# Optimization experiments

Hardware: AMD Instinct MI355X
Metric: run time of the kernel (lower is better)

Reference implementation:

```python
import jax, jax.numpy as jnp
import numpy as np

N, R, H0, H1, NB, E = 25000, 16, 256, 256, 16, 800000


def setup_inputs() -> dict:
    key = jax.random.key(0)
    ks = jax.random.split(key, 6)
    s = jax.random.randint(ks[0], (E,), 0, N)
    p = jax.random.randint(ks[1], (E,), 0, R)
    o = jax.random.randint(ks[2], (E,), 0, N)
    triples = jnp.stack([s, p, o], axis=1)  # (E, 3) int
    nodes = jax.random.normal(ks[3], (N, H0), dtype=jnp.float32)
    xav_c = (6.0 / (R + NB)) ** 0.5  # xavier-uniform scale proxy
    xav_b = (6.0 / (H0 + H1)) ** 0.5
    comps = jax.random.uniform(ks[4], (R, NB), dtype=jnp.float32, minval=-xav_c, maxval=xav_c)
    bases = jax.random.uniform(ks[5], (NB, H0, H1), dtype=jnp.float32, minval=-xav_b, maxval=xav_b)
    bias = jnp.zeros((H1,), dtype=jnp.float32)
    return {"triples": triples, "nodes": nodes, "comps": comps, "bases": bases, "bias": bias}


def reference(triples, nodes, comps, bases, bias):
    # RGCNLayer forward, hor=True, decomp='basis', insize given.
    s, p, o = triples[:, 0], triples[:, 1], triples[:, 2]
    e = s.shape[0]
    # Vertical adjacency row index (p*n + s); normalization = 1 / row-sum (sum_sparse)
    row_ver = p * N + s
    deg = jax.ops.segment_sum(jnp.ones((e,), dtype=nodes.dtype), row_ver, num_segments=R * N)
    vals = 1.0 / deg[row_ver]  # (E,) per-edge normalized value
    # Basis decomposition: weights (R, H0, H1)
    weights = jnp.einsum('rb,bij->rij', comps, bases)
    # Horizontal path: nw[r, n] = nodes @ W_r, then out = hor_adj @ nw.reshape(R*N, H1)
    nw = jnp.einsum('ni,rio->rno', nodes, weights)  # (R, N, H1)
    msgs = vals[:, None] * nw[p, o]  # (E, H1) gather of column blocks (p*n + o)
    out = jax.ops.segment_sum(msgs, s, num_segments=N)  # (N, H1) scatter into rows s
    return out + bias
```

## Files before the change

kernel.cpp:

```cpp
#include <hip/hip_runtime.h>
#include <hip/hip_bf16.h>

#define NN 25000
#define RR 16
#define H0 256
#define H1 256
#define NBASE 16
#define EE 800000
#define NKEY (NN*RR)
#define NKEY_PAD 400384
#define SCAN_NB 391

#define BM 32
#define CAPE 2048

static const size_t CNT_OFF  = 0;
static const size_t CUR_OFF  = 1601536;
static const size_t OFFS_OFF = 3203072;
static const size_t PART_OFF = 4804608;
static const size_t PERM_OFF = 4806656;
static const size_t W2_OFF   = 8006656;

typedef short bf16x8 __attribute__((ext_vector_type(8)));
typedef float f32x4  __attribute__((ext_vector_type(4)));

static __device__ __forceinline__ unsigned short f2bf(float f) {
    union { float f; unsigned u; } v; v.f = f;
    unsigned x = v.u;
    return (unsigned short)((x + 0x7FFFu + ((x >> 16) & 1u)) >> 16);
}

__global__ __launch_bounds__(256) void k_weights(const float* __restrict__ comps,
                                                 const float* __restrict__ bases,
                                                 unsigned short* __restrict__ W2) {
    __shared__ float sc[RR * NBASE];
    int t = threadIdx.x;
    sc[t] = comps[t];
    __syncthreads();
    int i = blockIdx.x;
    int j = t;
    int ij = i * 256 + j;
    float bv[NBASE];
#pragma unroll
    for (int b = 0; b < NBASE; ++b) bv[b] = bases[b * H0 * H1 + ij];
    int ks = i >> 5, u = i & 7, lq = (i >> 3) & 3;
    int nb = j >> 4, ln = j & 15;
#pragma unroll
    for (int r = 0; r < RR; ++r) {
        float acc = 0.f;
#pragma unroll
        for (int b = 0; b < NBASE; ++b) acc = fmaf(sc[r * NBASE + b], bv[b], acc);
        size_t sidx = (((size_t)(r * 8 + ks) * 16 + nb) * 64 + lq * 16 + ln) * 8 + u;
        W2[sidx] = f2bf(acc);
    }
}

__global__ __launch_bounds__(256) void k_cnt(const int* __restrict__ triples,
                                             int* __restrict__ cnt) {
    int e = blockIdx.x * 256 + threadIdx.x;
    if (e >= EE) return;
    int s = triples[3 * e];
    int p = triples[3 * e + 1];
    atomicAdd(&cnt[s * RR + p], 1);
}

__global__ __launch_bounds__(256) void k_scan1(const int* __restrict__ cnt,
                                               int* __restrict__ part) {
    __shared__ int sh[256];
    int t = threadIdx.x;
    int4 v = *(const int4*)(cnt + blockIdx.x * 1024 + t * 4);
    sh[t] = v.x + v.y + v.z + v.w;
    __syncthreads();
    for (int off = 128; off > 0; off >>= 1) {
        if (t < off) sh[t] += sh[t + off];
        __syncthreads();
    }
    if (t == 0) part[blockIdx.x] = sh[0];
}

__global__ void k_scan2(int* __restrict__ part) {
    __shared__ int sh[512];
    int t = threadIdx.x;
    sh[t] = (t < SCAN_NB) ? part[t] : 0;
    __syncthreads();
    for (int off = 1; off < 512; off <<= 1) {
        int v = (t >= off) ? sh[t - off] : 0;
        __syncthreads();
        sh[t] += v;
        __syncthreads();
    }
    if (t < SCAN_NB) part[t] = (t ? sh[t - 1] : 0);
}

__global__ __launch_bounds__(256) void k_scan3(const int* __restrict__ cnt,
                                               const int* __restrict__ part,
                                               int* __restrict__ offs) {
    __shared__ int sh[256];
    int t = threadIdx.x;
    int base = blockIdx.x * 1024 + t * 4;
    int4 v = *(const int4*)(cnt + base);
    sh[t] = v.x + v.y + v.z + v.w;
    __syncthreads();
    for (int off = 1; off < 256; off <<= 1) {
        int x = (t >= off) ? sh[t - off] : 0;
        __syncthreads();
        sh[t] += x;
        __syncthreads();
    }
    int texcl = part[blockIdx.x] + (t ? sh[t - 1] : 0);
    int4 w;
    w.x = texcl;
    w.y = texcl + v.x;
    w.z = texcl + v.x + v.y;
    w.w = texcl + v.x + v.y + v.z;
    *(int4*)(offs + base) = w;
}

__global__ __launch_bounds__(256) void k_fill(const int* __restrict__ triples,
                                              const int* __restrict__ offs,
                                              int* __restrict__ cur,
                                              int* __restrict__ perm_o) {
    int e = blockIdx.x * 256 + threadIdx.x;
    if (e >= EE) return;
    int s = triples[3 * e];
    int p = triples[3 * e + 1];
    int o = triples[3 * e + 2];
    int key = s * RR + p;
    int slot = offs[key] + atomicAdd(&cur[key], 1);
    perm_o[slot] = o;
}

__global__ __launch_bounds__(256, 4) void k_fused(const float* __restrict__ nodes,
                                                  const unsigned short* __restrict__ W2,
                                                  const int* __restrict__ offs,
                                                  const int* __restrict__ perm_o,
                                                  const float* __restrict__ bias,
                                                  float* __restrict__ out) {
    __shared__ int offs_l[BM * RR + 1];
    __shared__ int eo[CAPE];
    __shared__ unsigned short As[BM][264];

    int t = threadIdx.x;
    int l = t & 63;
    int w = t >> 6;
    int m0 = blockIdx.x * BM;
    int key0 = m0 * RR;

    for (int idx = t; idx < BM * RR + 1; idx += 256) {
        int g = key0 + idx;
        if (g > NKEY_PAD - 1) g = NKEY_PAD - 1;
        offs_l[idx] = offs[g];
    }
    __syncthreads();
    int base0 = offs_l[0];
    int span  = offs_l[BM * RR] - base0;
    for (int j = t; j < span && j < CAPE; j += 256) eo[j] = perm_o[base0 + j];
    __syncthreads();

    f32x4 acc[2][4];
#pragma unroll
    for (int mi = 0; mi < 2; ++mi)
#pragma unroll
        for (int ni = 0; ni < 4; ++ni) acc[mi][ni] = (f32x4){0.f, 0.f, 0.f, 0.f};

    for (int p = 0; p < RR; ++p) {
#pragma unroll
        for (int i = 0; i < 8; ++i) {
            int m = w * 8 + i;
            int s = m0 + m;
            float sx = 0.f, sy = 0.f, sz = 0.f, sw = 0.f;
            int c = 0;
            if (s < NN) {
                int loc = m * RR + p;
                int b = offs_l[loc] - base0;
                c = offs_l[loc + 1] - offs_l[loc];
                int j2 = 0;
                for (; j2 + 1 < c; j2 += 2) {
                    int x1 = b + j2, x2 = b + j2 + 1;
                    int o1 = (x1 < CAPE) ? eo[x1] : perm_o[base0 + x1];
                    int o2 = (x2 < CAPE) ? eo[x2] : perm_o[base0 + x2];
                    float4 v1 = *(const float4*)(nodes + (size_t)o1 * H0 + l * 4);
                    float4 v2 = *(const float4*)(nodes + (size_t)o2 * H0 + l * 4);
                    sx += v1.x + v2.x; sy += v1.y + v2.y;
                    sz += v1.z + v2.z; sw += v1.w + v2.w;
                }
                if (j2 < c) {
                    int x1 = b + j2;
                    int o1 = (x1 < CAPE) ? eo[x1] : perm_o[base0 + x1];
                    float4 v1 = *(const float4*)(nodes + (size_t)o1 * H0 + l * 4);
                    sx += v1.x; sy += v1.y; sz += v1.z; sw += v1.w;
                }
            }
            float inv = c ? 1.f / (float)c : 0.f;
            ushort4 pk;
            pk.x = f2bf(sx * inv); pk.y = f2bf(sy * inv);
            pk.z = f2bf(sz * inv); pk.w = f2bf(sw * inv);
            *(ushort4*)&As[m][l * 4] = pk;
        }
        __syncthreads();

        const unsigned short* Wp = W2 + (size_t)p * 65536;
#pragma unroll
        for (int ks = 0; ks < 8; ++ks) {
            int k0 = ks * 32;
            bf16x8 a0 = *(const bf16x8*)&As[(l & 15)][k0 + (l >> 4) * 8];
            bf16x8 a1 = *(const bf16x8*)&As[16 + (l & 15)][k0 + (l >> 4) * 8];
            const unsigned short* wb = Wp + ((size_t)ks * 16 + w * 4) * 512 + (size_t)l * 8;
            bf16x8 b0 = *(const bf16x8*)(wb);
            bf16x8 b1 = *(const bf16x8*)(wb + 512);
            bf16x8 b2 = *(const bf16x8*)(wb + 1024);
            bf16x8 b3 = *(const bf16x8*)(wb + 1536);
            acc[0][0] = __builtin_amdgcn_mfma_f32_16x16x32_bf16(a0, b0, acc[0][0], 0, 0, 0);
            acc[1][0] = __builtin_amdgcn_mfma_f32_16x16x32_bf16(a1, b0, acc[1][0], 0, 0, 0);
            acc[0][1] = __builtin_amdgcn_mfma_f32_16x16x32_bf16(a0, b1, acc[0][1], 0, 0, 0);
            acc[1][1] = __builtin_amdgcn_mfma_f32_16x16x32_bf16(a1, b1, acc[1][1], 0, 0, 0);
            acc[0][2] = __builtin_amdgcn_mfma_f32_16x16x32_bf16(a0, b2, acc[0][2], 0, 0, 0);
            acc[1][2] = __builtin_amdgcn_mfma_f32_16x16x32_bf16(a1, b2, acc[1][2], 0, 0, 0);
            acc[0][3] = __builtin_amdgcn_mfma_f32_16x16x32_bf16(a0, b3, acc[0][3], 0, 0, 0);
            acc[1][3] = __builtin_amdgcn_mfma_f32_16x16x32_bf16(a1, b3, acc[1][3], 0, 0, 0);
        }
        __syncthreads();
    }

    int colbase = w * 64 + (l & 15);
    float bl[4];
#pragma unroll
    for (int ni = 0; ni < 4; ++ni) bl[ni] = bias[colbase + ni * 16];
#pragma unroll
    for (int mi = 0; mi < 2; ++mi)
#pragma unroll
        for (int j = 0; j < 4; ++j) {
            int row = m0 + mi * 16 + (l >> 4) * 4 + j;
            if (row < NN) {
#pragma unroll
                for (int ni = 0; ni < 4; ++ni)
                    out[(size_t)row * H1 + colbase + ni * 16] = acc[mi][ni][j] + bl[ni];
            }
        }
}

extern "C" void kernel_launch(void* const* d_in, const int* in_sizes, int n_in,
                              void* d_out, int out_size, void* d_ws, size_t ws_size,
                              hipStream_t stream) {
    const int*   triples = (const int*)d_in[0];
    const float* nodes   = (const float*)d_in[1];
    const float* comps   = (const float*)d_in[2];
    const float* bases   = (const float*)d_in[3];
    const float* bias    = (const float*)d_in[4];
    float* out = (float*)d_out;

    char* ws = (char*)d_ws;
    int*            cnt    = (int*)(ws + CNT_OFF);
    int*            cur    = (int*)(ws + CUR_OFF);
    int*            offs   = (int*)(ws + OFFS_OFF);
    int*            part   = (int*)(ws + PART_OFF);
    int*            perm_o = (int*)(ws + PERM_OFF);
    unsigned short* W2     = (unsigned short*)(ws + W2_OFF);

    hipMemsetAsync(ws + CNT_OFF, 0, CUR_OFF + 1601536, stream);

    k_weights<<<256, 256, 0, stream>>>(comps, bases, W2);
    k_cnt<<<(EE + 255) / 256, 256, 0, stream>>>(triples, cnt);
    k_scan1<<<SCAN_NB, 256, 0, stream>>>(cnt, part);
    k_scan2<<<1, 512, 0, stream>>>(part);
    k_scan3<<<SCAN_NB, 256, 0, stream>>>(cnt, part, offs);
    k_fill<<<(EE + 255) / 256, 256, 0, stream>>>(triples, offs, cur, perm_o);
    k_fused<<<(NN + BM - 1) / BM, 256, 0, stream>>>(nodes, W2, offs, perm_o, bias, out);
}
```

Before: 357.7 us.

## Double-buffer aggregation with MFMA, halve row tile, reuse counts in fill

```diff
diff --git a/kernel.cpp b/kernel.cpp
--- a/kernel.cpp
+++ b/kernel.cpp
@@ -11,8 +11,8 @@
 #define NKEY_PAD 400384
 #define SCAN_NB 391
 
-#define BM 32
-#define CAPE 2048
+#define BM 16
+#define CAPE 1024
 
 static const size_t CNT_OFF  = 0;
 static const size_t CUR_OFF  = 1601536;
@@ -118,7 +118,7 @@
 
 __global__ __launch_bounds__(256) void k_fill(const int* __restrict__ triples,
                                               const int* __restrict__ offs,
-                                              int* __restrict__ cur,
+                                              int* __restrict__ cnt,
                                               int* __restrict__ perm_o) {
     int e = blockIdx.x * 256 + threadIdx.x;
     if (e >= EE) return;
@@ -126,11 +126,11 @@
     int p = triples[3 * e + 1];
     int o = triples[3 * e + 2];
     int key = s * RR + p;
-    int slot = offs[key] + atomicAdd(&cur[key], 1);
-    perm_o[slot] = o;
-}
-
-__global__ __launch_bounds__(256, 4) void k_fused(const float* __restrict__ nodes,
+    int r = atomicSub(&cnt[key], 1) - 1;
+    perm_o[offs[key] + r] = o;
+}
+
+__global__ __launch_bounds__(256, 6) void k_fused(const float* __restrict__ nodes,
                                                   const unsigned short* __restrict__ W2,
                                                   const int* __restrict__ offs,
                                                   const int* __restrict__ perm_o,
@@ -138,7 +138,7 @@
                                                   float* __restrict__ out) {
     __shared__ int offs_l[BM * RR + 1];
     __shared__ int eo[CAPE];
-    __shared__ unsigned short As[BM][264];
+    __shared__ unsigned short As[2][BM][264];
 
     int t = threadIdx.x;
     int l = t & 63;
@@ -155,18 +155,15 @@
     int base0 = offs_l[0];
     int span  = offs_l[BM * RR] - base0;
     for (int j = t; j < span && j < CAPE; j += 256) eo[j] = perm_o[base0 + j];
-    __syncthreads();
-
-    f32x4 acc[2][4];
-#pragma unroll
-    for (int mi = 0; mi < 2; ++mi)
-#pragma unroll
-        for (int ni = 0; ni < 4; ++ni) acc[mi][ni] = (f32x4){0.f, 0.f, 0.f, 0.f};
-
-    for (int p = 0; p < RR; ++p) {
-#pragma unroll
-        for (int i = 0; i < 8; ++i) {
-            int m = w * 8 + i;
+
+    f32x4 acc[4];
+#pragma unroll
+    for (int ni = 0; ni < 4; ++ni) acc[ni] = (f32x4){0.f, 0.f, 0.f, 0.f};
+
+    auto aggregate = [&](int p, int buf) {
+#pragma unroll
+        for (int i = 0; i < 4; ++i) {
+            int m = w * 4 + i;
             int s = m0 + m;
             float sx = 0.f, sy = 0.f, sz = 0.f, sw = 0.f;
             int c = 0;
@@ -195,29 +192,30 @@
             ushort4 pk;
             pk.x = f2bf(sx * inv); pk.y = f2bf(sy * inv);
             pk.z = f2bf(sz * inv); pk.w = f2bf(sw * inv);
-            *(ushort4*)&As[m][l * 4] = pk;
+            *(ushort4*)&As[buf][m][l * 4] = pk;
         }
-        __syncthreads();
-
+    };
+
+    __syncthreads();
+    aggregate(0, 0);
+    __syncthreads();
+
+    for (int p = 0; p < RR; ++p) {
+        if (p + 1 < RR) aggregate(p + 1, (p + 1) & 1);
+        int cb = p & 1;
         const unsigned short* Wp = W2 + (size_t)p * 65536;
 #pragma unroll
         for (int ks = 0; ks < 8; ++ks) {
-            int k0 = ks * 32;
-            bf16x8 a0 = *(const bf16x8*)&As[(l & 15)][k0 + (l >> 4) * 8];
-            bf16x8 a1 = *(const bf16x8*)&As[16 + (l & 15)][k0 + (l >> 4) * 8];
+            bf16x8 a0 = *(const bf16x8*)&As[cb][(l & 15)][ks * 32 + (l >> 4) * 8];
             const unsigned short* wb = Wp + ((size_t)ks * 16 + w * 4) * 512 + (size_t)l * 8;
             bf16x8 b0 = *(const bf16x8*)(wb);
             bf16x8 b1 = *(const bf16x8*)(wb + 512);
             bf16x8 b2 = *(const bf16x8*)(wb + 1024);
             bf16x8 b3 = *(const bf16x8*)(wb + 1536);
-            acc[0][0] = __builtin_amdgcn_mfma_f32_16x16x32_bf16(a0, b0, acc[0][0], 0, 0, 0);
-            acc[1][0] = __builtin_amdgcn_mfma_f32_16x16x32_bf16(a1, b0, acc[1][0], 0, 0, 0);
-            acc[0][1] = __builtin_amdgcn_mfma_f32_16x16x32_bf16(a0, b1, acc[0][1], 0, 0, 0);
-            acc[1][1] = __builtin_amdgcn_mfma_f32_16x16x32_bf16(a1, b1, acc[1][1], 0, 0, 0);
-            acc[0][2] = __builtin_amdgcn_mfma_f32_16x16x32_bf16(a0, b2, acc[0][2], 0, 0, 0);
-            acc[1][2] = __builtin_amdgcn_mfma_f32_16x16x32_bf16(a1, b2, acc[1][2], 0, 0, 0);
-            acc[0][3] = __builtin_amdgcn_mfma_f32_16x16x32_bf16(a0, b3, acc[0][3], 0, 0, 0);
-            acc[1][3] = __builtin_amdgcn_mfma_f32_16x16x32_bf16(a1, b3, acc[1][3], 0, 0, 0);
+            acc[0] = __builtin_amdgcn_mfma_f32_16x16x32_bf16(a0, b0, acc[0], 0, 0, 0);
+            acc[1] = __builtin_amdgcn_mfma_f32_16x16x32_bf16(a0, b1, acc[1], 0, 0, 0);
+            acc[2] = __builtin_amdgcn_mfma_f32_16x16x32_bf16(a0, b2, acc[2], 0, 0, 0);
+            acc[3] = __builtin_amdgcn_mfma_f32_16x16x32_bf16(a0, b3, acc[3], 0, 0, 0);
         }
         __syncthreads();
     }
@@ -227,16 +225,14 @@
 #pragma unroll
     for (int ni = 0; ni < 4; ++ni) bl[ni] = bias[colbase + ni * 16];
 #pragma unroll
-    for (int mi = 0; mi < 2; ++mi)
-#pragma unroll
-        for (int j = 0; j < 4; ++j) {
-            int row = m0 + mi * 16 + (l >> 4) * 4 + j;
-            if (row < NN) {
-#pragma unroll
-                for (int ni = 0; ni < 4; ++ni)
-                    out[(size_t)row * H1 + colbase + ni * 16] = acc[mi][ni][j] + bl[ni];
-            }
+    for (int j = 0; j < 4; ++j) {
+        int row = m0 + (l >> 4) * 4 + j;
+        if (row < NN) {
+#pragma unroll
+            for (int ni = 0; ni < 4; ++ni)
+                out[(size_t)row * H1 + colbase + ni * 16] = acc[ni][j] + bl[ni];
         }
+    }
 }
 
 extern "C" void kernel_launch(void* const* d_in, const int* in_sizes, int n_in,
@@ -251,19 +247,18 @@
 
     char* ws = (char*)d_ws;
     int*            cnt    = (int*)(ws + CNT_OFF);
-    int*            cur    = (int*)(ws + CUR_OFF);
     int*            offs   = (int*)(ws + OFFS_OFF);
     int*            part   = (int*)(ws + PART_OFF);
     int*            perm_o = (int*)(ws + PERM_OFF);
     unsigned short* W2     = (unsigned short*)(ws + W2_OFF);
 
-    hipMemsetAsync(ws + CNT_OFF, 0, CUR_OFF + 1601536, stream);
+    hipMemsetAsync(ws + CNT_OFF, 0, 1601536, stream);
 
     k_weights<<<256, 256, 0, stream>>>(comps, bases, W2);
     k_cnt<<<(EE + 255) / 256, 256, 0, stream>>>(triples, cnt);
     k_scan1<<<SCAN_NB, 256, 0, stream>>>(cnt, part);
     k_scan2<<<1, 512, 0, stream>>>(part);
     k_scan3<<<SCAN_NB, 256, 0, stream>>>(cnt, part, offs);
-    k_fill<<<(EE + 255) / 256, 256, 0, stream>>>(triples, offs, cur, perm_o);
+    k_fill<<<(EE + 255) / 256, 256, 0, stream>>>(triples, offs, cnt, perm_o);
     k_fused<<<(NN + BM - 1) / BM, 256, 0, stream>>>(nodes, W2, offs, perm_o, bias, out);
 }
```

Result: no change. 363.5 us (+1.6%).

## Gather bf16 node features, double-buffer aggregation tile, reuse counts for fill

Applied to the files above, without the earlier changes.

```diff
diff --git a/kernel.cpp b/kernel.cpp
--- a/kernel.cpp
+++ b/kernel.cpp
@@ -15,13 +15,14 @@
 #define CAPE 2048
 
 static const size_t CNT_OFF  = 0;
-static const size_t CUR_OFF  = 1601536;
-static const size_t OFFS_OFF = 3203072;
-static const size_t PART_OFF = 4804608;
-static const size_t PERM_OFF = 4806656;
-static const size_t W2_OFF   = 8006656;
+static const size_t OFFS_OFF = 1601536;
+static const size_t PART_OFF = 3203072;
+static const size_t PERM_OFF = 3205120;
+static const size_t W2_OFF   = 6405120;
+static const size_t NBF_OFF  = 8502272;
 
 typedef short bf16x8 __attribute__((ext_vector_type(8)));
+typedef short short8 __attribute__((ext_vector_type(8)));
 typedef float f32x4  __attribute__((ext_vector_type(4)));
 
 static __device__ __forceinline__ unsigned short f2bf(float f) {
@@ -29,6 +30,9 @@
     unsigned x = v.u;
     return (unsigned short)((x + 0x7FFFu + ((x >> 16) & 1u)) >> 16);
 }
+static __device__ __forceinline__ float b2f(unsigned short u) {
+    union { unsigned u; float f; } v; v.u = ((unsigned)u) << 16; return v.f;
+}
 
 __global__ __launch_bounds__(256) void k_weights(const float* __restrict__ comps,
                                                  const float* __restrict__ bases,
@@ -55,13 +59,26 @@
     }
 }
 
-__global__ __launch_bounds__(256) void k_cnt(const int* __restrict__ triples,
-                                             int* __restrict__ cnt) {
-    int e = blockIdx.x * 256 + threadIdx.x;
-    if (e >= EE) return;
-    int s = triples[3 * e];
-    int p = triples[3 * e + 1];
-    atomicAdd(&cnt[s * RR + p], 1);
+#define CVT_NB 3125
+__global__ __launch_bounds__(256) void k_prep(const float* __restrict__ nodes,
+                                              const int* __restrict__ triples,
+                                              unsigned short* __restrict__ nbf,
+                                              int* __restrict__ cnt) {
+    int b = blockIdx.x;
+    if (b < CVT_NB) {
+        int i = b * 2048 + threadIdx.x * 8;
+        float4 v0 = *(const float4*)(nodes + i);
+        float4 v1 = *(const float4*)(nodes + i + 4);
+        short8 pk;
+        pk[0] = f2bf(v0.x); pk[1] = f2bf(v0.y); pk[2] = f2bf(v0.z); pk[3] = f2bf(v0.w);
+        pk[4] = f2bf(v1.x); pk[5] = f2bf(v1.y); pk[6] = f2bf(v1.z); pk[7] = f2bf(v1.w);
+        *(short8*)(nbf + i) = pk;
+    } else {
+        int e = (b - CVT_NB) * 256 + threadIdx.x;
+        int s = triples[3 * e];
+        int p = triples[3 * e + 1];
+        atomicAdd(&cnt[s * RR + p], 1);
+    }
 }
 
 __global__ __launch_bounds__(256) void k_scan1(const int* __restrict__ cnt,
@@ -118,7 +135,7 @@
 
 __global__ __launch_bounds__(256) void k_fill(const int* __restrict__ triples,
                                               const int* __restrict__ offs,
-                                              int* __restrict__ cur,
+                                              int* __restrict__ cnt,
                                               int* __restrict__ perm_o) {
     int e = blockIdx.x * 256 + threadIdx.x;
     if (e >= EE) return;
@@ -126,11 +143,11 @@
     int p = triples[3 * e + 1];
     int o = triples[3 * e + 2];
     int key = s * RR + p;
-    int slot = offs[key] + atomicAdd(&cur[key], 1);
-    perm_o[slot] = o;
-}
-
-__global__ __launch_bounds__(256, 4) void k_fused(const float* __restrict__ nodes,
+    int r = atomicSub(&cnt[key], 1) - 1;
+    perm_o[offs[key] + r] = o;
+}
+
+__global__ __launch_bounds__(256, 4) void k_fused(const unsigned short* __restrict__ nbf,
                                                   const unsigned short* __restrict__ W2,
                                                   const int* __restrict__ offs,
                                                   const int* __restrict__ perm_o,
@@ -138,7 +155,7 @@
                                                   float* __restrict__ out) {
     __shared__ int offs_l[BM * RR + 1];
     __shared__ int eo[CAPE];
-    __shared__ unsigned short As[BM][264];
+    __shared__ unsigned short As[2][BM][264];
 
     int t = threadIdx.x;
     int l = t & 63;
@@ -155,7 +172,6 @@
     int base0 = offs_l[0];
     int span  = offs_l[BM * RR] - base0;
     for (int j = t; j < span && j < CAPE; j += 256) eo[j] = perm_o[base0 + j];
-    __syncthreads();
 
     f32x4 acc[2][4];
 #pragma unroll
@@ -163,7 +179,7 @@
 #pragma unroll
         for (int ni = 0; ni < 4; ++ni) acc[mi][ni] = (f32x4){0.f, 0.f, 0.f, 0.f};
 
-    for (int p = 0; p < RR; ++p) {
+    auto aggregate = [&](int p, int buf) {
 #pragma unroll
         for (int i = 0; i < 8; ++i) {
             int m = w * 8 + i;
@@ -179,32 +195,39 @@
                     int x1 = b + j2, x2 = b + j2 + 1;
                     int o1 = (x1 < CAPE) ? eo[x1] : perm_o[base0 + x1];
                     int o2 = (x2 < CAPE) ? eo[x2] : perm_o[base0 + x2];
-                    float4 v1 = *(const float4*)(nodes + (size_t)o1 * H0 + l * 4);
-                    float4 v2 = *(const float4*)(nodes + (size_t)o2 * H0 + l * 4);
-                    sx += v1.x + v2.x; sy += v1.y + v2.y;
-                    sz += v1.z + v2.z; sw += v1.w + v2.w;
+                    ushort4 v1 = *(const ushort4*)(nbf + (size_t)o1 * H0 + l * 4);
+                    ushort4 v2 = *(const ushort4*)(nbf + (size_t)o2 * H0 + l * 4);
+                    sx += b2f(v1.x) + b2f(v2.x); sy += b2f(v1.y) + b2f(v2.y);
+                    sz += b2f(v1.z) + b2f(v2.z); sw += b2f(v1.w) + b2f(v2.w);
                 }
                 if (j2 < c) {
                     int x1 = b + j2;
                     int o1 = (x1 < CAPE) ? eo[x1] : perm_o[base0 + x1];
-                    float4 v1 = *(const float4*)(nodes + (size_t)o1 * H0 + l * 4);
-                    sx += v1.x; sy += v1.y; sz += v1.z; sw += v1.w;
+                    ushort4 v1 = *(const ushort4*)(nbf + (size_t)o1 * H0 + l * 4);
+                    sx += b2f(v1.x); sy += b2f(v1.y); sz += b2f(v1.z); sw += b2f(v1.w);
                 }
             }
             float inv = c ? 1.f / (float)c : 0.f;
             ushort4 pk;
             pk.x = f2bf(sx * inv); pk.y = f2bf(sy * inv);
             pk.z = f2bf(sz * inv); pk.w = f2bf(sw * inv);
-            *(ushort4*)&As[m][l * 4] = pk;
+            *(ushort4*)&As[buf][m][l * 4] = pk;
         }
-        __syncthreads();
-
+    };
+
+    __syncthreads();
+    aggregate(0, 0);
+    __syncthreads();
+
+    for (int p = 0; p < RR; ++p) {
+        if (p + 1 < RR) aggregate(p + 1, (p + 1) & 1);
+        int cb = p & 1;
         const unsigned short* Wp = W2 + (size_t)p * 65536;
 #pragma unroll
         for (int ks = 0; ks < 8; ++ks) {
             int k0 = ks * 32;
-            bf16x8 a0 = *(const bf16x8*)&As[(l & 15)][k0 + (l >> 4) * 8];
-            bf16x8 a1 = *(const bf16x8*)&As[16 + (l & 15)][k0 + (l >> 4) * 8];
+            bf16x8 a0 = *(const bf16x8*)&As[cb][(l & 15)][k0 + (l >> 4) * 8];
+            bf16x8 a1 = *(const bf16x8*)&As[cb][16 + (l & 15)][k0 + (l >> 4) * 8];
             const unsigned short* wb = Wp + ((size_t)ks * 16 + w * 4) * 512 + (size_t)l * 8;
             bf16x8 b0 = *(const bf16x8*)(wb);
             bf16x8 b1 = *(const bf16x8*)(wb + 512);
@@ -251,19 +274,19 @@
 
     char* ws = (char*)d_ws;
     int*            cnt    = (int*)(ws + CNT_OFF);
-    int*            cur    = (int*)(ws + CUR_OFF);
     int*            offs   = (int*)(ws + OFFS_OFF);
     int*            part   = (int*)(ws + PART_OFF);
     int*            perm_o = (int*)(ws + PERM_OFF);
     unsigned short* W2     = (unsigned short*)(ws + W2_OFF);
-
-    hipMemsetAsync(ws + CNT_OFF, 0, CUR_OFF + 1601536, stream);
+    unsigned short* nbf    = (unsigned short*)(ws + NBF_OFF);
+
+    hipMemsetAsync(ws + CNT_OFF, 0, 1601536, stream);
 
     k_weights<<<256, 256, 0, stream>>>(comps, bases, W2);
-    k_cnt<<<(EE + 255) / 256, 256, 0, stream>>>(triples, cnt);
+    k_prep<<<CVT_NB + EE / 256, 256, 0, stream>>>(nodes, triples, nbf, cnt);
     k_scan1<<<SCAN_NB, 256, 0, stream>>>(cnt, part);
     k_scan2<<<1, 512, 0, stream>>>(part);
     k_scan3<<<SCAN_NB, 256, 0, stream>>>(cnt, part, offs);
-    k_fill<<<(EE + 255) / 256, 256, 0, stream>>>(triples, offs, cur, perm_o);
-    k_fused<<<(NN + BM - 1) / BM, 256, 0, stream>>>(nodes, W2, offs, perm_o, bias, out);
-}
+    k_fill<<<(EE + 255) / 256, 256, 0, stream>>>(triples, offs, cnt, perm_o);
+    k_fused<<<(NN + BM - 1) / BM, 256, 0, stream>>>(nbf, W2, offs, perm_o, bias, out);
+}
```

Result: slower. 475.1 us (+32.9%).
